# Optimization experiments

Measured on AMD Instinct MI355X. Metric: run time of the kernel, lower is better.

Reference implementation:

```python
import jax, jax.numpy as jnp
import numpy as np

N = 50000      # num nodes
E = 600000     # num edges (avg degree 12)
IN = 256       # in_feats
H = 128        # h_feats
P = 2          # prop_step
LN_EPS = 1e-5


def setup_inputs() -> dict:
    key = jax.random.key(0)
    ks = jax.random.split(key, 8)
    return {
        "in_feat": jax.random.normal(ks[0], (N, IN), jnp.float32),
        "row": jax.random.randint(ks[1], (E,), 0, N),  # target node of each edge
        "col": jax.random.randint(ks[2], (E,), 0, N),  # source node of each edge
        "lin_w": jax.random.normal(ks[3], (H, IN), jnp.float32) / np.sqrt(IN).astype(np.float32),
        "lin_b": jnp.zeros((H,), jnp.float32),
        "conv_w": jax.random.normal(ks[4], (H, H), jnp.float32) / np.sqrt(H).astype(np.float32),
        "conv_b": jnp.zeros((H,), jnp.float32),
        "root_emb": jax.random.normal(ks[5], (1, H), jnp.float32) * 0.02,
        "ln_gamma": jnp.ones((P, H), jnp.float32),
        "ln_beta": jnp.zeros((P, H), jnp.float32),
    }


def _layernorm(x, g, b):
    mu = jnp.mean(x, axis=-1, keepdims=True)
    var = jnp.mean(jnp.square(x - mu), axis=-1, keepdims=True)
    return (x - mu) * jax.lax.rsqrt(var + LN_EPS) * g + b


def reference(in_feat, row, col, lin_w, lin_b, conv_w, conv_b, root_emb, ln_gamma, ln_beta):
    n = in_feat.shape[0]
    h = in_feat @ lin_w.T + lin_b                      # [N, H]

    # OGB-style degree norm with +1 trick (original edges, row = target)
    deg = jax.ops.segment_sum(jnp.ones_like(row, dtype=h.dtype), row, num_segments=n) + 1.0
    deg_inv = 1.0 / deg                                # deg >= 1, never inf

    # GCNConv symmetric norm with self loops: D^-1/2 (A+I) D^-1/2
    loop = jnp.arange(n)
    r2 = jnp.concatenate([row, loop])                  # [E+N] targets
    c2 = jnp.concatenate([col, loop])                  # [E+N] sources
    d2 = jax.ops.segment_sum(jnp.ones_like(r2, dtype=h.dtype), r2, num_segments=n)
    dis = jnp.where(d2 > 0, jax.lax.rsqrt(jnp.maximum(d2, 1.0)), 0.0)
    ew = dis[r2] * dis[c2]                             # [E+N] edge weights

    root = root_emb[0]                                 # [H]
    ori = h
    for i in range(P):
        if i != 0:
            h = h + ori                                # residual
            h = _layernorm(h, ln_gamma[i], ln_beta[i])
            h = jax.nn.relu(h)
            # dropout=0.0 -> identity
        xw = h @ conv_w.T                              # [N, H]
        h_msg = jax.ops.segment_sum(ew[:, None] * xw[c2], r2, num_segments=n) + conv_b
        root_contrib = jax.nn.relu(h + root) * deg_inv[:, None]
        h = h_msg + root_contrib
    return h
```

## Files before the change

### kernel.cpp

```cpp
#include <hip/hip_runtime.h>
#include <stdint.h>

#define NN 50000
#define EE 600000
#define INF 256
#define HF 128
#define CEB ((EE + 255) / 256)
#define GBT ((NN + 63) / 64)
#define NBCH ((NN + 255) / 256)

typedef __attribute__((ext_vector_type(8))) short short8;
typedef __attribute__((ext_vector_type(4))) float floatx4;

__device__ __forceinline__ unsigned short f32_to_bf16_rne(float x) {
    unsigned int u = __float_as_uint(x);
    unsigned int r = (u + 0x7FFFu + ((u >> 16) & 1u)) >> 16;
    return (unsigned short)r;
}
__device__ __forceinline__ float bf16_to_f32(unsigned short h) {
    return __uint_as_float(((unsigned int)h) << 16);
}
__device__ __forceinline__ float bf16lo_u32(unsigned int u) {
    return __uint_as_float(u << 16);
}
__device__ __forceinline__ float bf16hi_u32(unsigned int u) {
    return __uint_as_float(u & 0xFFFF0000u);
}
__device__ __forceinline__ void cvt_hilo8(float4 v0, float4 v1, short8& hs, short8& ls) {
    float x[8] = {v0.x, v0.y, v0.z, v0.w, v1.x, v1.y, v1.z, v1.w};
    union { short8 s; unsigned short u[8]; } H, L;
#pragma unroll
    for (int k = 0; k < 8; ++k) {
        unsigned short hi = f32_to_bf16_rne(x[k]);
        H.u[k] = hi;
        L.u[k] = f32_to_bf16_rne(x[k] - bf16_to_f32(hi));
    }
    hs = H.s;
    ls = L.s;
}

__device__ __forceinline__ void prepack_one(int idx, const float* lw, const float* cw,
                                            unsigned short* fl, unsigned short* fc) {
    const float* src; unsigned short* dst; int K, c;
    if (idx < 8192) { src = lw; dst = fl; K = INF; c = idx; }
    else            { src = cw; dst = fc; K = HF; c = idx - 8192; }
    int lane = c & 63;
    int nt = (c >> 6) & 7;
    int hl = (c >> 9) & 1;
    int kc = c >> 10;
    int rw = nt * 16 + (lane & 15);
    int koff = kc * 32 + (lane >> 4) * 8;
    const float* p = &src[(size_t)rw * K + koff];
    float4 v0 = *reinterpret_cast<const float4*>(p);
    float4 v1 = *reinterpret_cast<const float4*>(p + 4);
    short8 hs, ls;
    cvt_hilo8(v0, v1, hs, ls);
    *reinterpret_cast<short8*>(&dst[(size_t)c * 8]) = hl ? ls : hs;
}

__global__ void zero_prepack(const float* __restrict__ lw, const float* __restrict__ cw,
                             unsigned short* __restrict__ fl, unsigned short* __restrict__ fc,
                             int* __restrict__ cnt, int* __restrict__ done_ctr) {
    int g = blockIdx.x * 256 + threadIdx.x;
    if (g < 12288) prepack_one(g, lw, cw, fl, fc);
    for (int i = g; i < NN; i += 256 * 256) cnt[i] = 0;
    if (g == 0) *done_ctr = 0;
}

__global__ void scan_all(const int* __restrict__ cnt, int* __restrict__ bsum,
                         int* __restrict__ done_ctr, int* __restrict__ row_start,
                         float* __restrict__ deg_inv, float* __restrict__ dis) {
    __shared__ int sdata[256];
    __shared__ int eb[256];
    __shared__ int flag;
    int c = blockIdx.x, t = threadIdx.x;
    int i = c * 256 + t;
    int v = (i < NN) ? cnt[i] : 0;
    sdata[t] = v;
    __syncthreads();
    for (int s = 1; s < 256; s <<= 1) {
        int add = (t >= s) ? sdata[t - s] : 0;
        __syncthreads();
        sdata[t] += add;
        __syncthreads();
    }
    if (i < NN) {
        row_start[i] = sdata[t] - v;
        float d = (float)(v + 1);
        deg_inv[i] = 1.0f / d;
        dis[i] = rsqrtf(d);
    }
    if (t == 255) bsum[c] = sdata[255];
    __syncthreads();
    if (t == 0) {
        __threadfence();
        flag = (atomicAdd(done_ctr, 1) == NBCH - 1);
    }
    __syncthreads();
    if (!flag) return;
    __threadfence();
    int bv = (t < NBCH) ? bsum[t] : 0;
    sdata[t] = bv;
    __syncthreads();
    for (int s = 1; s < 256; s <<= 1) {
        int add = (t >= s) ? sdata[t - s] : 0;
        __syncthreads();
        sdata[t] += add;
        __syncthreads();
    }
    eb[t] = sdata[t] - bv;
    __syncthreads();
    for (int j = t; j < NN; j += 256) row_start[j] += eb[j >> 8];
    if (t == 0) row_start[NN] = EE;
}

template <int K, int MODE>
__device__ __forceinline__ void gemm_tile(
    int bidx, const float* __restrict__ Af, const unsigned short* __restrict__ Wf,
    const float* __restrict__ bias, float* __restrict__ Cf,
    unsigned short* __restrict__ Chi, unsigned short* __restrict__ Clo,
    unsigned short* WS, int M) {
    constexpr int NKC = K / 32;
    const int t = threadIdx.x;
    const int wave = t >> 6;
    const int lane = t & 63;
    const int lrow = lane & 15;
    const int quad = lane >> 4;
    const int bm = bidx * 64;
    int arow = bm + wave * 16 + lrow;
    if (arow >= M) arow = M - 1;

    floatx4 acc[8];
#pragma unroll
    for (int nt = 0; nt < 8; ++nt) acc[nt] = (floatx4){0.f, 0.f, 0.f, 0.f};

#pragma unroll
    for (int pp = 0; pp < NKC / 2; ++pp) {
        if (pp) __syncthreads();
        {
            const unsigned short* src = Wf + (size_t)pp * 16384 + (size_t)t * 8;
#if __has_builtin(__builtin_amdgcn_global_load_lds)
#pragma unroll
            for (int i = 0; i < 8; ++i) {
                __builtin_amdgcn_global_load_lds(
                    (const unsigned int*)(src + (size_t)i * 2048),
                    (unsigned int*)(WS + ((size_t)i * 256 + (t >> 6) * 64) * 8),
                    16, 0, 0);
            }
#else
            const uint4* s4 = reinterpret_cast<const uint4*>(Wf + (size_t)pp * 16384);
            uint4* d4 = reinterpret_cast<uint4*>(WS);
#pragma unroll
            for (int i = 0; i < 8; ++i) d4[t + 256 * i] = s4[t + 256 * i];
#endif
        }
        __syncthreads();
#pragma unroll
        for (int k2 = 0; k2 < 2; ++k2) {
            int kc = pp * 2 + k2;
            const float* ap = &Af[(size_t)arow * K + kc * 32 + quad * 8];
            float4 a0 = *reinterpret_cast<const float4*>(ap);
            float4 a1 = *reinterpret_cast<const float4*>(ap + 4);
            short8 afh, afl;
            cvt_hilo8(a0, a1, afh, afl);
            const unsigned short* wb = &WS[k2 * 8192 + lane * 8];
#pragma unroll
            for (int nt = 0; nt < 8; ++nt) {
                short8 bfh = *reinterpret_cast<const short8*>(wb + nt * 512);
                short8 bfl = *reinterpret_cast<const short8*>(wb + 4096 + nt * 512);
                acc[nt] = __builtin_amdgcn_mfma_f32_16x16x32_bf16(afh, bfh, acc[nt], 0, 0, 0);
                acc[nt] = __builtin_amdgcn_mfma_f32_16x16x32_bf16(afl, bfh, acc[nt], 0, 0, 0);
                acc[nt] = __builtin_amdgcn_mfma_f32_16x16x32_bf16(afh, bfl, acc[nt], 0, 0, 0);
            }
        }
    }

    float cb[8];
    if (MODE == 0) {
#pragma unroll
        for (int nt = 0; nt < 8; ++nt) cb[nt] = bias[nt * 16 + lrow];
    }

#pragma unroll
    for (int r = 0; r < 4; ++r) {
        int grow = bm + wave * 16 + quad * 4 + r;
        if (grow >= M) continue;
#pragma unroll
        for (int nt = 0; nt < 8; ++nt) {
            int colh = nt * 16 + lrow;
            if (MODE == 0) {
                Cf[(size_t)grow * HF + colh] = acc[nt][r] + cb[nt];
            } else {
                float x = acc[nt][r];
                unsigned short hi = f32_to_bf16_rne(x);
                Chi[(size_t)grow * HF + colh] = hi;
                Clo[(size_t)grow * HF + colh] = f32_to_bf16_rne(x - bf16_to_f32(hi));
            }
        }
    }
}

__global__ __launch_bounds__(256) void gemm0_count(
    const float* __restrict__ in_feat, const unsigned short* __restrict__ fl,
    const float* __restrict__ lin_b, float* __restrict__ h0,
    const int* __restrict__ row, int* __restrict__ cnt, int* __restrict__ pos) {
    __shared__ unsigned short WS[2 * 8192];
    int b = blockIdx.x;
    if (b < GBT) {
        gemm_tile<INF, 0>(b, in_feat, fl, lin_b, h0, nullptr, nullptr, WS, NN);
        return;
    }
    int e = (b - GBT) * 256 + threadIdx.x;
    if (e < EE) pos[e] = atomicAdd(&cnt[row[e]], 1);
}

__global__ __launch_bounds__(256) void xw_fill(
    const float* __restrict__ h, const unsigned short* __restrict__ fc,
    unsigned short* __restrict__ xw_hi, unsigned short* __restrict__ xw_lo,
    const int* __restrict__ row, const int* __restrict__ col,
    const int* __restrict__ row_start, const int* __restrict__ pos,
    int* __restrict__ csr_col) {
    __shared__ unsigned short WS[2 * 8192];
    int b = blockIdx.x;
    if (b < GBT) {
        gemm_tile<HF, 1>(b, h, fc, nullptr, nullptr, xw_hi, xw_lo, WS, NN);
        return;
    }
    int e = (b - GBT) * 256 + threadIdx.x;
    if (e < EE) {
        int p = row_start[row[e]] + pos[e];
        __builtin_nontemporal_store(col[e], &csr_col[p]);
    }
}

__global__ __launch_bounds__(256) void xw_only(
    const float* __restrict__ h, const unsigned short* __restrict__ fc,
    unsigned short* __restrict__ xw_hi, unsigned short* __restrict__ xw_lo) {
    __shared__ unsigned short WS[2 * 8192];
    gemm_tile<HF, 1>(blockIdx.x, h, fc, nullptr, nullptr, xw_hi, xw_lo, WS, NN);
}

template <int STEP>
__global__ void agg_ep(const int* __restrict__ row_start, const int* __restrict__ csr_col,
                       const float* __restrict__ dis, const float* __restrict__ deg_inv,
                       const unsigned short* __restrict__ xw_hi,
                       const unsigned short* __restrict__ xw_lo,
                       const float* __restrict__ conv_b, const float* __restrict__ root,
                       const float* __restrict__ gamma, const float* __restrict__ beta,
                       float* __restrict__ h, float* __restrict__ outp, int n) {
    int wid = (blockIdx.x * blockDim.x + threadIdx.x) >> 6;
    int lane = threadIdx.x & 63;
    if (wid >= n) return;
    int q = lane >> 4;
    int l16 = lane & 15;
    int s = row_start[wid];
    int e = row_start[wid + 1];
    float a0 = 0.f, a1 = 0.f, a2 = 0.f, a3 = 0.f, a4 = 0.f, a5 = 0.f, a6 = 0.f, a7 = 0.f;
    if (e - s <= 16) {
        int j0 = s + q;
        bool p0 = j0 < e, p1 = j0 + 4 < e, p2 = j0 + 8 < e, p3 = j0 + 12 < e;
        int c0 = p0 ? csr_col[j0] : 0;
        int c1 = p1 ? csr_col[j0 + 4] : 0;
        int c2 = p2 ? csr_col[j0 + 8] : 0;
        int c3 = p3 ? csr_col[j0 + 12] : 0;
        float d0 = dis[c0], d1 = dis[c1], d2 = dis[c2], d3 = dis[c3];
        uint4 z = make_uint4(0, 0, 0, 0);
        uint4 g0 = z, g1 = z, g2 = z, g3 = z;
        if (p0) g0 = *reinterpret_cast<const uint4*>(&xw_hi[(size_t)c0 * HF + l16 * 8]);
        if (p1) g1 = *reinterpret_cast<const uint4*>(&xw_hi[(size_t)c1 * HF + l16 * 8]);
        if (p2) g2 = *reinterpret_cast<const uint4*>(&xw_hi[(size_t)c2 * HF + l16 * 8]);
        if (p3) g3 = *reinterpret_cast<const uint4*>(&xw_hi[(size_t)c3 * HF + l16 * 8]);
        a0 = d0 * bf16lo_u32(g0.x) + d1 * bf16lo_u32(g1.x) + d2 * bf16lo_u32(g2.x) + d3 * bf16lo_u32(g3.x);
        a1 = d0 * bf16hi_u32(g0.x) + d1 * bf16hi_u32(g1.x) + d2 * bf16hi_u32(g2.x) + d3 * bf16hi_u32(g3.x);
        a2 = d0 * bf16lo_u32(g0.y) + d1 * bf16lo_u32(g1.y) + d2 * bf16lo_u32(g2.y) + d3 * bf16lo_u32(g3.y);
        a3 = d0 * bf16hi_u32(g0.y) + d1 * bf16hi_u32(g1.y) + d2 * bf16hi_u32(g2.y) + d3 * bf16hi_u32(g3.y);
        a4 = d0 * bf16lo_u32(g0.z) + d1 * bf16lo_u32(g1.z) + d2 * bf16lo_u32(g2.z) + d3 * bf16lo_u32(g3.z);
        a5 = d0 * bf16hi_u32(g0.z) + d1 * bf16hi_u32(g1.z) + d2 * bf16hi_u32(g2.z) + d3 * bf16hi_u32(g3.z);
        a6 = d0 * bf16lo_u32(g0.w) + d1 * bf16lo_u32(g1.w) + d2 * bf16lo_u32(g2.w) + d3 * bf16lo_u32(g3.w);
        a7 = d0 * bf16hi_u32(g0.w) + d1 * bf16hi_u32(g1.w) + d2 * bf16hi_u32(g2.w) + d3 * bf16hi_u32(g3.w);
    } else {
        float b0 = 0.f, b1 = 0.f, b2 = 0.f, b3 = 0.f, b4 = 0.f, b5 = 0.f, b6 = 0.f, b7 = 0.f;
        int j = s + q;
        for (; j + 4 < e; j += 8) {
            int c0 = csr_col[j];
            int c1 = csr_col[j + 4];
            float d0 = dis[c0];
            float d1 = dis[c1];
            uint4 h0v = *reinterpret_cast<const uint4*>(&xw_hi[(size_t)c0 * HF + l16 * 8]);
            uint4 h1v = *reinterpret_cast<const uint4*>(&xw_hi[(size_t)c1 * HF + l16 * 8]);
            a0 = fmaf(d0, bf16lo_u32(h0v.x), a0); a1 = fmaf(d0, bf16hi_u32(h0v.x), a1);
            a2 = fmaf(d0, bf16lo_u32(h0v.y), a2); a3 = fmaf(d0, bf16hi_u32(h0v.y), a3);
            a4 = fmaf(d0, bf16lo_u32(h0v.z), a4); a5 = fmaf(d0, bf16hi_u32(h0v.z), a5);
            a6 = fmaf(d0, bf16lo_u32(h0v.w), a6); a7 = fmaf(d0, bf16hi_u32(h0v.w), a7);
            b0 = fmaf(d1, bf16lo_u32(h1v.x), b0); b1 = fmaf(d1, bf16hi_u32(h1v.x), b1);
            b2 = fmaf(d1, bf16lo_u32(h1v.y), b2); b3 = fmaf(d1, bf16hi_u32(h1v.y), b3);
            b4 = fmaf(d1, bf16lo_u32(h1v.z), b4); b5 = fmaf(d1, bf16hi_u32(h1v.z), b5);
            b6 = fmaf(d1, bf16lo_u32(h1v.w), b6); b7 = fmaf(d1, bf16hi_u32(h1v.w), b7);
        }
        if (j < e) {
            int c0 = csr_col[j];
            float d0 = dis[c0];
            uint4 h0v = *reinterpret_cast<const uint4*>(&xw_hi[(size_t)c0 * HF + l16 * 8]);
            a0 = fmaf(d0, bf16lo_u32(h0v.x), a0); a1 = fmaf(d0, bf16hi_u32(h0v.x), a1);
            a2 = fmaf(d0, bf16lo_u32(h0v.y), a2); a3 = fmaf(d0, bf16hi_u32(h0v.y), a3);
            a4 = fmaf(d0, bf16lo_u32(h0v.z), a4); a5 = fmaf(d0, bf16hi_u32(h0v.z), a5);
            a6 = fmaf(d0, bf16lo_u32(h0v.w), a6); a7 = fmaf(d0, bf16hi_u32(h0v.w), a7);
        }
        a0 += b0; a1 += b1; a2 += b2; a3 += b3;
        a4 += b4; a5 += b5; a6 += b6; a7 += b7;
    }
#pragma unroll
    for (int m = 16; m < 64; m <<= 1) {
        a0 += __shfl_xor(a0, m, 64);
        a1 += __shfl_xor(a1, m, 64);
        a2 += __shfl_xor(a2, m, 64);
        a3 += __shfl_xor(a3, m, 64);
        a4 += __shfl_xor(a4, m, 64);
        a5 += __shfl_xor(a5, m, 64);
        a6 += __shfl_xor(a6, m, 64);
        a7 += __shfl_xor(a7, m, 64);
    }
    if (q != 0) return;
    float av[8] = {a0, a1, a2, a3, a4, a5, a6, a7};
    int f = l16 * 8;
    float dn = dis[wid];
    float di = deg_inv[wid];
    uint4 xh = *reinterpret_cast<const uint4*>(&xw_hi[(size_t)wid * HF + f]);
    uint4 xl = *reinterpret_cast<const uint4*>(&xw_lo[(size_t)wid * HF + f]);
    float sf[8];
    sf[0] = bf16lo_u32(xh.x) + bf16lo_u32(xl.x);
    sf[1] = bf16hi_u32(xh.x) + bf16hi_u32(xl.x);
    sf[2] = bf16lo_u32(xh.y) + bf16lo_u32(xl.y);
    sf[3] = bf16hi_u32(xh.y) + bf16hi_u32(xl.y);
    sf[4] = bf16lo_u32(xh.z) + bf16lo_u32(xl.z);
    sf[5] = bf16hi_u32(xh.z) + bf16hi_u32(xl.z);
    sf[6] = bf16lo_u32(xh.w) + bf16lo_u32(xl.w);
    sf[7] = bf16hi_u32(xh.w) + bf16hi_u32(xl.w);
    float4 hA = *reinterpret_cast<const float4*>(&h[(size_t)wid * HF + f]);
    float4 hB = *reinterpret_cast<const float4*>(&h[(size_t)wid * HF + f + 4]);
    float hv[8] = {hA.x, hA.y, hA.z, hA.w, hB.x, hB.y, hB.z, hB.w};
    float v[8];
#pragma unroll
    for (int k = 0; k < 8; ++k) {
        float msg = fmaf(dn, av[k], di * sf[k]) + conv_b[f + k];
        v[k] = msg + fmaxf(hv[k] + root[f + k], 0.f) * di;
    }
    if (STEP == 0) {
        float x[8];
        float ssum = 0.f;
#pragma unroll
        for (int k = 0; k < 8; ++k) { x[k] = v[k] + hv[k]; ssum += x[k]; }
#pragma unroll
        for (int m = 1; m < 16; m <<= 1) ssum += __shfl_xor(ssum, m, 64);
        float mu = ssum * (1.0f / HF);
        float var = 0.f;
#pragma unroll
        for (int k = 0; k < 8; ++k) { float d = x[k] - mu; var += d * d; }
#pragma unroll
        for (int m = 1; m < 16; m <<= 1) var += __shfl_xor(var, m, 64);
        float rs = rsqrtf(var * (1.0f / HF) + 1e-5f);
        float y[8];
#pragma unroll
        for (int k = 0; k < 8; ++k)
            y[k] = fmaxf((x[k] - mu) * rs * gamma[f + k] + beta[f + k], 0.f);
        *reinterpret_cast<float4*>(&h[(size_t)wid * HF + f]) =
            make_float4(y[0], y[1], y[2], y[3]);
        *reinterpret_cast<float4*>(&h[(size_t)wid * HF + f + 4]) =
            make_float4(y[4], y[5], y[6], y[7]);
    } else {
        *reinterpret_cast<float4*>(&outp[(size_t)wid * HF + f]) =
            make_float4(v[0], v[1], v[2], v[3]);
        *reinterpret_cast<float4*>(&outp[(size_t)wid * HF + f + 4]) =
            make_float4(v[4], v[5], v[6], v[7]);
    }
}

extern "C" void kernel_launch(void* const* d_in, const int* in_sizes, int n_in,
                              void* d_out, int out_size, void* d_ws, size_t ws_size,
                              hipStream_t stream) {
    const int N = NN;
    const float* in_feat = (const float*)d_in[0];
    const int* row = (const int*)d_in[1];
    const int* col = (const int*)d_in[2];
    const float* lin_w = (const float*)d_in[3];
    const float* lin_b = (const float*)d_in[4];
    const float* conv_w = (const float*)d_in[5];
    const float* conv_b = (const float*)d_in[6];
    const float* root_emb = (const float*)d_in[7];
    const float* ln_gamma = (const float*)d_in[8];
    const float* ln_beta = (const float*)d_in[9];
    float* out = (float*)d_out;

    float* ws = (float*)d_ws;
    size_t o = 0;
    float* deg_inv = ws + o; o += N;
    float* dis = ws + o; o += N;
    int* cnt = (int*)(ws + o); o += N;
    int* row_start = (int*)(ws + o); o += N + 4;
    int* pos = (int*)(ws + o); o += EE;
    int* bsum = (int*)(ws + o); o += 256;
    int* done_ctr = (int*)(ws + o); o += 4;
    int* csr_col = (int*)(ws + o); o += EE;
    unsigned short* fl = (unsigned short*)(ws + o); o += 32768;
    unsigned short* fc = (unsigned short*)(ws + o); o += 16384;
    float* h0 = ws + o; o += (size_t)N * HF;
    unsigned short* xw_hi = (unsigned short*)(ws + o); o += (size_t)N * HF / 2;
    unsigned short* xw_lo = (unsigned short*)(ws + o); o += (size_t)N * HF / 2;

    const int WB = (N + 3) / 4;

    zero_prepack<<<256, 256, 0, stream>>>(lin_w, conv_w, fl, fc, cnt, done_ctr);
    gemm0_count<<<GBT + CEB, 256, 0, stream>>>(in_feat, fl, lin_b, h0, row, cnt, pos);
    scan_all<<<NBCH, 256, 0, stream>>>(cnt, bsum, done_ctr, row_start, deg_inv, dis);
    xw_fill<<<GBT + CEB, 256, 0, stream>>>(h0, fc, xw_hi, xw_lo,
                                           row, col, row_start, pos, csr_col);
    agg_ep<0><<<WB, 256, 0, stream>>>(row_start, csr_col, dis, deg_inv, xw_hi, xw_lo,
                                      conv_b, root_emb, ln_gamma + HF, ln_beta + HF,
                                      h0, nullptr, N);
    xw_only<<<GBT, 256, 0, stream>>>(h0, fc, xw_hi, xw_lo);
    agg_ep<1><<<WB, 256, 0, stream>>>(row_start, csr_col, dis, deg_inv, xw_hi, xw_lo,
                                      conv_b, root_emb, nullptr, nullptr,
                                      h0, out, N);
}
```

Baseline: 292.0 us.

## Privatize degree counters into eight lanes and split scan into two kernels

Edge-degree counting now spreads atomics across eight private counter arrays, chosen by edge-block index, to cut contention on the same node counter. The scan is rebuilt as a block-sum kernel followed by a kernel that redoes the block-sum prefix and writes per-lane CSR offsets, which replaces the last-block atomic done-counter scheme. CSR fill reads the per-lane offsets directly. The cost is eight times the counter memory to zero and read, plus one extra kernel launch.

```diff
diff --git a/kernel.cpp b/kernel.cpp
--- a/kernel.cpp
+++ b/kernel.cpp
@@ -8,6 +8,7 @@
 #define CEB ((EE + 255) / 256)
 #define GBT ((NN + 63) / 64)
 #define NBCH ((NN + 255) / 256)
+#define NLB 8
 
 typedef __attribute__((ext_vector_type(8))) short short8;
 typedef __attribute__((ext_vector_type(4))) float floatx4;
@@ -60,22 +61,56 @@
 
 __global__ void zero_prepack(const float* __restrict__ lw, const float* __restrict__ cw,
                              unsigned short* __restrict__ fl, unsigned short* __restrict__ fc,
-                             int* __restrict__ cnt, int* __restrict__ done_ctr) {
+                             int* __restrict__ cnt8) {
     int g = blockIdx.x * 256 + threadIdx.x;
     if (g < 12288) prepack_one(g, lw, cw, fl, fc);
-    for (int i = g; i < NN; i += 256 * 256) cnt[i] = 0;
-    if (g == 0) *done_ctr = 0;
-}
-
-__global__ void scan_all(const int* __restrict__ cnt, int* __restrict__ bsum,
-                         int* __restrict__ done_ctr, int* __restrict__ row_start,
-                         float* __restrict__ deg_inv, float* __restrict__ dis) {
+    for (int i = g; i < NLB * NN; i += 256 * 256) cnt8[i] = 0;
+}
+
+__global__ void scan_phase1(const int* __restrict__ cnt8, int* __restrict__ bsum, int n) {
     __shared__ int sdata[256];
-    __shared__ int eb[256];
-    __shared__ int flag;
-    int c = blockIdx.x, t = threadIdx.x;
-    int i = c * 256 + t;
-    int v = (i < NN) ? cnt[i] : 0;
+    int t = threadIdx.x;
+    int i = blockIdx.x * 256 + t;
+    int d = 0;
+    if (i < n) {
+#pragma unroll
+        for (int k = 0; k < NLB; ++k) d += cnt8[(size_t)k * NN + i];
+    }
+    sdata[t] = d;
+    __syncthreads();
+    for (int s = 128; s > 0; s >>= 1) {
+        if (t < s) sdata[t] += sdata[t + s];
+        __syncthreads();
+    }
+    if (t == 0) bsum[blockIdx.x] = sdata[0];
+}
+
+__global__ void scan_phase3(int* __restrict__ cnt8, const int* __restrict__ bsum,
+                            int* __restrict__ row_start,
+                            float* __restrict__ deg_inv, float* __restrict__ dis,
+                            int n, int nb, int E) {
+    __shared__ int sb[256];
+    __shared__ int sdata[256];
+    int t = threadIdx.x;
+    sb[t] = (t < nb) ? bsum[t] : 0;
+    __syncthreads();
+    for (int s = 1; s < 256; s <<= 1) {
+        int add = (t >= s) ? sb[t - s] : 0;
+        __syncthreads();
+        sb[t] += add;
+        __syncthreads();
+    }
+    int base = sb[blockIdx.x] - bsum[blockIdx.x];
+    int i = blockIdx.x * 256 + t;
+    int c8[NLB];
+    int v = 0;
+    if (i < n) {
+#pragma unroll
+        for (int k = 0; k < NLB; ++k) {
+            c8[k] = cnt8[(size_t)k * NN + i];
+            v += c8[k];
+        }
+    }
     sdata[t] = v;
     __syncthreads();
     for (int s = 1; s < 256; s <<= 1) {
@@ -84,34 +119,21 @@
         sdata[t] += add;
         __syncthreads();
     }
-    if (i < NN) {
-        row_start[i] = sdata[t] - v;
+    if (i < n) {
+        int rs = base + sdata[t] - v;
+        row_start[i] = rs;
+        int acc = rs;
+#pragma unroll
+        for (int k = 0; k < NLB; ++k) {
+            int cc = c8[k];
+            cnt8[(size_t)k * NN + i] = acc;
+            acc += cc;
+        }
         float d = (float)(v + 1);
         deg_inv[i] = 1.0f / d;
         dis[i] = rsqrtf(d);
     }
-    if (t == 255) bsum[c] = sdata[255];
-    __syncthreads();
-    if (t == 0) {
-        __threadfence();
-        flag = (atomicAdd(done_ctr, 1) == NBCH - 1);
-    }
-    __syncthreads();
-    if (!flag) return;
-    __threadfence();
-    int bv = (t < NBCH) ? bsum[t] : 0;
-    sdata[t] = bv;
-    __syncthreads();
-    for (int s = 1; s < 256; s <<= 1) {
-        int add = (t >= s) ? sdata[t - s] : 0;
-        __syncthreads();
-        sdata[t] += add;
-        __syncthreads();
-    }
-    eb[t] = sdata[t] - bv;
-    __syncthreads();
-    for (int j = t; j < NN; j += 256) row_start[j] += eb[j >> 8];
-    if (t == 0) row_start[NN] = EE;
+    if (blockIdx.x == 0 && t == 0) row_start[n] = E;
 }
 
 template <int K, int MODE>
@@ -203,22 +225,23 @@
 __global__ __launch_bounds__(256) void gemm0_count(
     const float* __restrict__ in_feat, const unsigned short* __restrict__ fl,
     const float* __restrict__ lin_b, float* __restrict__ h0,
-    const int* __restrict__ row, int* __restrict__ cnt, int* __restrict__ pos) {
+    const int* __restrict__ row, int* __restrict__ cnt8, int* __restrict__ pos) {
     __shared__ unsigned short WS[2 * 8192];
     int b = blockIdx.x;
     if (b < GBT) {
         gemm_tile<INF, 0>(b, in_feat, fl, lin_b, h0, nullptr, nullptr, WS, NN);
         return;
     }
-    int e = (b - GBT) * 256 + threadIdx.x;
-    if (e < EE) pos[e] = atomicAdd(&cnt[row[e]], 1);
+    int eb = b - GBT;
+    int e = eb * 256 + threadIdx.x;
+    if (e < EE) pos[e] = atomicAdd(&cnt8[(size_t)(eb & 7) * NN + row[e]], 1);
 }
 
 __global__ __launch_bounds__(256) void xw_fill(
     const float* __restrict__ h, const unsigned short* __restrict__ fc,
     unsigned short* __restrict__ xw_hi, unsigned short* __restrict__ xw_lo,
     const int* __restrict__ row, const int* __restrict__ col,
-    const int* __restrict__ row_start, const int* __restrict__ pos,
+    const int* __restrict__ cnt8_base, const int* __restrict__ pos,
     int* __restrict__ csr_col) {
     __shared__ unsigned short WS[2 * 8192];
     int b = blockIdx.x;
@@ -226,9 +249,10 @@
         gemm_tile<HF, 1>(b, h, fc, nullptr, nullptr, xw_hi, xw_lo, WS, NN);
         return;
     }
-    int e = (b - GBT) * 256 + threadIdx.x;
+    int eb = b - GBT;
+    int e = eb * 256 + threadIdx.x;
     if (e < EE) {
-        int p = row_start[row[e]] + pos[e];
+        int p = cnt8_base[(size_t)(eb & 7) * NN + row[e]] + pos[e];
         __builtin_nontemporal_store(col[e], &csr_col[p]);
     }
 }
@@ -378,7 +402,7 @@
 extern "C" void kernel_launch(void* const* d_in, const int* in_sizes, int n_in,
                               void* d_out, int out_size, void* d_ws, size_t ws_size,
                               hipStream_t stream) {
-    const int N = NN;
+    const int N = NN, E = EE;
     const float* in_feat = (const float*)d_in[0];
     const int* row = (const int*)d_in[1];
     const int* col = (const int*)d_in[2];
@@ -395,12 +419,11 @@
     size_t o = 0;
     float* deg_inv = ws + o; o += N;
     float* dis = ws + o; o += N;
-    int* cnt = (int*)(ws + o); o += N;
+    int* cnt8 = (int*)(ws + o); o += (size_t)NLB * N;
     int* row_start = (int*)(ws + o); o += N + 4;
-    int* pos = (int*)(ws + o); o += EE;
+    int* pos = (int*)(ws + o); o += E;
     int* bsum = (int*)(ws + o); o += 256;
-    int* done_ctr = (int*)(ws + o); o += 4;
-    int* csr_col = (int*)(ws + o); o += EE;
+    int* csr_col = (int*)(ws + o); o += E;
     unsigned short* fl = (unsigned short*)(ws + o); o += 32768;
     unsigned short* fc = (unsigned short*)(ws + o); o += 16384;
     float* h0 = ws + o; o += (size_t)N * HF;
@@ -409,11 +432,12 @@
 
     const int WB = (N + 3) / 4;
 
-    zero_prepack<<<256, 256, 0, stream>>>(lin_w, conv_w, fl, fc, cnt, done_ctr);
-    gemm0_count<<<GBT + CEB, 256, 0, stream>>>(in_feat, fl, lin_b, h0, row, cnt, pos);
-    scan_all<<<NBCH, 256, 0, stream>>>(cnt, bsum, done_ctr, row_start, deg_inv, dis);
+    zero_prepack<<<256, 256, 0, stream>>>(lin_w, conv_w, fl, fc, cnt8);
+    gemm0_count<<<GBT + CEB, 256, 0, stream>>>(in_feat, fl, lin_b, h0, row, cnt8, pos);
+    scan_phase1<<<NBCH, 256, 0, stream>>>(cnt8, bsum, N);
+    scan_phase3<<<NBCH, 256, 0, stream>>>(cnt8, bsum, row_start, deg_inv, dis, N, NBCH, E);
     xw_fill<<<GBT + CEB, 256, 0, stream>>>(h0, fc, xw_hi, xw_lo,
-                                           row, col, row_start, pos, csr_col);
+                                           row, col, cnt8, pos, csr_col);
     agg_ep<0><<<WB, 256, 0, stream>>>(row_start, csr_col, dis, deg_inv, xw_hi, xw_lo,
                                       conv_b, root_emb, ln_gamma + HF, ln_beta + HF,
                                       h0, nullptr, N);
```

Measured after the change: 262.7 us. -10.0%, faster.
